# Kernel optimization log

Hardware: AMD Instinct MI355X
Metric: run time of the kernel (lower is better)

## Reference

```python
import jax, jax.numpy as jnp
import numpy as np


def _fft_feats(x):
    # x: [B, 3, H, W] float32
    B, C, H, W = x.shape
    gray = 0.299 * x[:, 0] + 0.587 * x[:, 1] + 0.114 * x[:, 2]  # [B,H,W]
    mag = jnp.abs(jnp.fft.fftshift(jnp.fft.fft2(gray), axes=(-2, -1))) + 1e-8
    mag = mag / (mag.max(axis=(-2, -1), keepdims=True) + 1e-8)
    m = mag.reshape(B, -1)
    n = m.shape[1]
    mean = m.mean(axis=1)
    std = jnp.clip(jnp.std(m, axis=1, ddof=1), 1e-8, None)  # torch unbiased std
    mx = m.max(axis=1)
    mn = m.min(axis=1)
    gt_mean = (m > mean[:, None]).astype(jnp.float32).mean(axis=1)
    # torch.median returns the lower of the two middle values for even n
    med = jnp.sort(m, axis=1)[:, (n - 1) // 2]
    q1 = mag[:, : H // 4].mean(axis=(1, 2))
    q2 = mag[:, H // 4 : H // 2].mean(axis=(1, 2))
    q3 = mag[:, H // 2 : 3 * H // 4].mean(axis=(1, 2))
    q4 = mag[:, 3 * H // 4 :].mean(axis=(1, 2))
    gt_half = (m > 0.5).astype(jnp.float32).mean(axis=1)
    gt_tenth = (m > 0.1).astype(jnp.float32).mean(axis=1)
    feats = jnp.stack([mean, std, mx, mn, gt_mean, med, q1, q2, q3, q4, gt_half, gt_tenth], axis=1)
    return jnp.clip(feats, -10.0, 10.0)  # [B,12]


def _bn(h, gamma, beta):
    # BatchNorm1d, training-mode forward (batch statistics, biased var), eps=1e-5
    mu = h.mean(axis=0)
    var = h.var(axis=0)
    return gamma * (h - mu) / jnp.sqrt(var + 1e-5) + beta


def _mlp(f, W1, b1, g1, be1, W2, b2, g2, be2, W3, b3):
    h = jax.nn.relu(_bn(f @ W1 + b1, g1, be1))  # Dropout(0.1) treated as identity (eval)
    h = jax.nn.relu(_bn(h @ W2 + b2, g2, be2))
    return h @ W3 + b3


def setup_inputs() -> dict:
    key = jax.random.key(0)
    ks = jax.random.split(key, 8)
    B, H, W = 64, 512, 512
    D = 512  # output_dim
    x = jax.random.normal(ks[0], (B, 3, H, W), dtype=jnp.float32)
    W1 = jax.random.normal(ks[1], (12, 64), dtype=jnp.float32) * 0.2
    b1 = jnp.zeros((64,), jnp.float32)
    g1 = jnp.ones((64,), jnp.float32)
    be1 = jnp.zeros((64,), jnp.float32)
    W2 = jax.random.normal(ks[2], (64, 128), dtype=jnp.float32) * 0.1
    b2 = jnp.zeros((128,), jnp.float32)
    g2 = jnp.ones((128,), jnp.float32)
    be2 = jnp.zeros((128,), jnp.float32)
    W3 = jax.random.normal(ks[3], (128, D), dtype=jnp.float32) * 0.08
    b3 = jnp.zeros((D,), jnp.float32)
    return {"x": x, "W1": W1, "b1": b1, "g1": g1, "be1": be1,
            "W2": W2, "b2": b2, "g2": g2, "be2": be2, "W3": W3, "b3": b3}


def reference(x, W1, b1, g1, be1, W2, b2, g2, be2, W3, b3):
    feats = _fft_feats(x)
    return _mlp(feats, W1, b1, g1, be1, W2, b2, g2, be2, W3, b3)
```

## Files before the change

kernel.cpp:

```cpp
#include <hip/hip_runtime.h>
#include <math.h>

#ifndef M_PI
#define M_PI 3.14159265358979323846
#endif

#define BB 64
#define HH 512
#define WW 512
#define NPIX (HH*WW)
#define MED_K 131072u
#define MAGB 131584
#define BSTRIDE 264
#define SS 520

__device__ __forceinline__ float wredf(float v){
  #pragma unroll
  for (int o = 32; o > 0; o >>= 1) v += __shfl_down(v, o, 64);
  return v;
}
__device__ __forceinline__ float wred_min(float v){
  #pragma unroll
  for (int o = 32; o > 0; o >>= 1) v = fminf(v, __shfl_down(v, o, 64));
  return v;
}
__device__ __forceinline__ float wred_max(float v){
  #pragma unroll
  for (int o = 32; o > 0; o >>= 1) v = fmaxf(v, __shfl_down(v, o, 64));
  return v;
}
__device__ __forceinline__ unsigned wred_addu(unsigned v){
  #pragma unroll
  for (int o = 32; o > 0; o >>= 1) v += __shfl_down(v, o, 64);
  return v;
}
__device__ __forceinline__ float wred_add_all(float v){
  #pragma unroll
  for (int o = 32; o > 0; o >>= 1) v += __shfl_xor(v, o, 64);
  return v;
}

__global__ void init_kernel(float2* __restrict__ twg, unsigned* __restrict__ scal){
  int t = threadIdx.x;
  double a = -2.0 * M_PI * (double)t / 512.0;
  twg[t] = make_float2((float)cos(a), (float)sin(a));
  #pragma unroll
  for (int q = 0; q < 8; ++q){
    int w = t*8 + q;
    scal[w] = (w >= 64 && w < 128) ? 0xFFFFFFFFu : 0u;
  }
}

__device__ __forceinline__ void build_twid(float2* T, const float2* __restrict__ twg,
                                           int t, int nthr){
  for (int i = t; i < 510; i += nthr){
    int v = i + 2;
    int z = 31 - __clz(v);
    T[i] = twg[(v - (1 << z)) << (8 - z)];
  }
}

__device__ __forceinline__ void wave_fft512(float (&re)[8], float (&im)[8],
                                            const float2* T, int lane){
  {
    const int d = 1;
    bool hi = (lane & d) != 0;
    #pragma unroll
    for (int r = 0; r < 8; ++r){
      float pre = __shfl_xor(re[r], d, 64);
      float pim = __shfl_xor(im[r], d, 64);
      float ur = hi ? pre : re[r], ui = hi ? pim : im[r];
      float vr = hi ? re[r] : pre, vi = hi ? im[r] : pim;
      re[r] = hi ? ur - vr : ur + vr;
      im[r] = hi ? ui - vi : ui + vi;
    }
  }
  #pragma unroll
  for (int st = 2; st <= 6; ++st){
    const int d = 1 << (st - 1);
    float2 w = T[((1 << (st - 1)) - 2) + (lane & (d - 1))];
    bool hi = (lane & d) != 0;
    #pragma unroll
    for (int r = 0; r < 8; ++r){
      float pre = __shfl_xor(re[r], d, 64);
      float pim = __shfl_xor(im[r], d, 64);
      float ur = hi ? pre : re[r], ui = hi ? pim : im[r];
      float rr = hi ? re[r] : pre, ri = hi ? im[r] : pim;
      float vr = w.x*rr - w.y*ri;
      float vi = w.x*ri + w.y*rr;
      re[r] = hi ? ur - vr : ur + vr;
      im[r] = hi ? ui - vi : ui + vi;
    }
  }
  {
    float2 w = T[62 + lane];
    #pragma unroll
    for (int r = 0; r < 8; r += 2){
      float vr = w.x*re[r+1] - w.y*im[r+1];
      float vi = w.x*im[r+1] + w.y*re[r+1];
      float ur = re[r], ui = im[r];
      re[r]   = ur + vr; im[r]   = ui + vi;
      re[r+1] = ur - vr; im[r+1] = ui - vi;
    }
  }
  {
    float2 w0 = T[126 + lane];
    float2 w1 = T[190 + lane];
    #pragma unroll
    for (int rb = 0; rb < 8; rb += 4){
      {
        float vr = w0.x*re[rb+2] - w0.y*im[rb+2];
        float vi = w0.x*im[rb+2] + w0.y*re[rb+2];
        float ur = re[rb], ui = im[rb];
        re[rb]   = ur + vr; im[rb]   = ui + vi;
        re[rb+2] = ur - vr; im[rb+2] = ui - vi;
      }
      {
        float vr = w1.x*re[rb+3] - w1.y*im[rb+3];
        float vi = w1.x*im[rb+3] + w1.y*re[rb+3];
        float ur = re[rb+1], ui = im[rb+1];
        re[rb+1] = ur + vr; im[rb+1] = ui + vi;
        re[rb+3] = ur - vr; im[rb+3] = ui - vi;
      }
    }
  }
  {
    #pragma unroll
    for (int r = 0; r < 4; ++r){
      float2 w = T[254 + 64*r + lane];
      float vr = w.x*re[r+4] - w.y*im[r+4];
      float vi = w.x*im[r+4] + w.y*re[r+4];
      float ur = re[r], ui = im[r];
      re[r]   = ur + vr; im[r]   = ui + vi;
      re[r+4] = ur - vr; im[r+4] = ui - vi;
    }
  }
}

__global__ __launch_bounds__(256) void row_fft_kernel(const float* __restrict__ x,
                                                      const float2* __restrict__ twg,
                                                      float2* __restrict__ out){
  __shared__ float2 T[510];
  int t = threadIdx.x;
  build_twid(T, twg, t, 256);
  __syncthreads();
  int lane = t & 63, wv = t >> 6;
  int pair = blockIdx.x*4 + wv;
  int b = pair >> 8, hp = pair & 255;
  int c0 = lane << 3;
  const float* p0 = x + (size_t)b*3*NPIX + (size_t)(2*hp)*WW + c0;
  const float* p1 = p0 + WW;
  float4 ra0 = *(const float4*)(p0);          float4 ra1 = *(const float4*)(p0+4);
  float4 ga0 = *(const float4*)(p0+NPIX);     float4 ga1 = *(const float4*)(p0+NPIX+4);
  float4 ba0 = *(const float4*)(p0+2*NPIX);   float4 ba1 = *(const float4*)(p0+2*NPIX+4);
  float4 rb0 = *(const float4*)(p1);          float4 rb1 = *(const float4*)(p1+4);
  float4 gb0 = *(const float4*)(p1+NPIX);     float4 gb1 = *(const float4*)(p1+NPIX+4);
  float4 bb0 = *(const float4*)(p1+2*NPIX);   float4 bb1 = *(const float4*)(p1+2*NPIX+4);
  float g0[8] = {0.299f*ra0.x + 0.587f*ga0.x + 0.114f*ba0.x,
                 0.299f*ra0.y + 0.587f*ga0.y + 0.114f*ba0.y,
                 0.299f*ra0.z + 0.587f*ga0.z + 0.114f*ba0.z,
                 0.299f*ra0.w + 0.587f*ga0.w + 0.114f*ba0.w,
                 0.299f*ra1.x + 0.587f*ga1.x + 0.114f*ba1.x,
                 0.299f*ra1.y + 0.587f*ga1.y + 0.114f*ba1.y,
                 0.299f*ra1.z + 0.587f*ga1.z + 0.114f*ba1.z,
                 0.299f*ra1.w + 0.587f*ga1.w + 0.114f*ba1.w};
  float g1[8] = {0.299f*rb0.x + 0.587f*gb0.x + 0.114f*bb0.x,
                 0.299f*rb0.y + 0.587f*gb0.y + 0.114f*bb0.y,
                 0.299f*rb0.z + 0.587f*gb0.z + 0.114f*bb0.z,
                 0.299f*rb0.w + 0.587f*gb0.w + 0.114f*bb0.w,
                 0.299f*rb1.x + 0.587f*gb1.x + 0.114f*bb1.x,
                 0.299f*rb1.y + 0.587f*gb1.y + 0.114f*bb1.y,
                 0.299f*rb1.z + 0.587f*gb1.z + 0.114f*bb1.z,
                 0.299f*rb1.w + 0.587f*gb1.w + 0.114f*bb1.w};
  int src = (int)(__brev((unsigned)lane) >> 26);
  float re[8], im[8];
  re[0] = __shfl(g0[0], src, 64); re[1] = __shfl(g0[4], src, 64);
  re[2] = __shfl(g0[2], src, 64); re[3] = __shfl(g0[6], src, 64);
  re[4] = __shfl(g0[1], src, 64); re[5] = __shfl(g0[5], src, 64);
  re[6] = __shfl(g0[3], src, 64); re[7] = __shfl(g0[7], src, 64);
  im[0] = __shfl(g1[0], src, 64); im[1] = __shfl(g1[4], src, 64);
  im[2] = __shfl(g1[2], src, 64); im[3] = __shfl(g1[6], src, 64);
  im[4] = __shfl(g1[1], src, 64); im[5] = __shfl(g1[5], src, 64);
  im[6] = __shfl(g1[3], src, 64); im[7] = __shfl(g1[7], src, 64);
  wave_fft512(re, im, T, lane);
  int row0 = (b << 9) + 2*hp;
  float2* o0 = out + (size_t)row0*BSTRIDE;
  float2* o1 = o0 + BSTRIDE;
  int srcl = (64 - lane) & 63;
  float p4r = __shfl(re[4], srcl, 64), p4i = __shfl(im[4], srcl, 64);
  float p5r = __shfl(re[5], srcl, 64), p5i = __shfl(im[5], srcl, 64);
  float p6r = __shfl(re[6], srcl, 64), p6i = __shfl(im[6], srcl, 64);
  float p7r = __shfl(re[7], srcl, 64), p7i = __shfl(im[7], srcl, 64);
  bool l0 = (lane == 0);
  {
    float zr = re[0], zi = im[0];
    float wr = l0 ? re[0] : p7r, wi = l0 ? im[0] : p7i;
    o0[lane] = make_float2(0.5f*(zr + wr), 0.5f*(zi - wi));
    o1[lane] = make_float2(0.5f*(zi + wi), 0.5f*(wr - zr));
  }
  {
    float zr = re[1], zi = im[1];
    float wr = l0 ? re[7] : p6r, wi = l0 ? im[7] : p6i;
    int k = lane + 64;
    o0[k] = make_float2(0.5f*(zr + wr), 0.5f*(zi - wi));
    o1[k] = make_float2(0.5f*(zi + wi), 0.5f*(wr - zr));
  }
  {
    float zr = re[2], zi = im[2];
    float wr = l0 ? re[6] : p5r, wi = l0 ? im[6] : p5i;
    int k = lane + 128;
    o0[k] = make_float2(0.5f*(zr + wr), 0.5f*(zi - wi));
    o1[k] = make_float2(0.5f*(zi + wi), 0.5f*(wr - zr));
  }
  {
    float zr = re[3], zi = im[3];
    float wr = l0 ? re[5] : p4r, wi = l0 ? im[5] : p4i;
    int k = lane + 192;
    o0[k] = make_float2(0.5f*(zr + wr), 0.5f*(zi - wi));
    o1[k] = make_float2(0.5f*(zi + wi), 0.5f*(wr - zr));
  }
  if (l0){
    float zr = re[4], zi = im[4];
    o0[256] = make_float2(zr, 0.f);
    o1[256] = make_float2(zi, 0.f);
  }
}

__global__ __launch_bounds__(512) void col_fft_kernel(const float2* __restrict__ in,
    const float2* __restrict__ twg,
    float* __restrict__ magc,
    unsigned* __restrict__ dmax, unsigned* __restrict__ dmin,
    double* __restrict__ sum, double* __restrict__ sumsq, double* __restrict__ qsum,
    unsigned* __restrict__ hist1)
{
  __shared__ float st_re[8*SS];
  __shared__ float st_im[8*SS];
  __shared__ float2 T[510];
  __shared__ unsigned h[8*256];
  __shared__ float buff[8][8];
  int t = threadIdx.x;
  int lane = t & 63, wv = t >> 6;
  build_twid(T, twg, t, 512);
  for (int i = t; i < 2048; i += 512) h[i] = 0u;
  int b = blockIdx.x / 33;
  int j0 = (blockIdx.x % 33) << 3;
  const float2* base = in + (size_t)b * (size_t)(512*BSTRIDE);
  #pragma unroll
  for (int it = 0; it < 8; ++it){
    int idx = t + (it << 9);
    int e = idx >> 3, jj = idx & 7;
    float2 v = base[(size_t)e*BSTRIDE + j0 + jj];
    int se = e ^ (e >> 3);
    st_re[jj*SS + se] = v.x;
    st_im[jj*SS + se] = v.y;
  }
  __syncthreads();
  int j = j0 + wv;
  if (j <= 256){
    int K = (int)(__brev((unsigned)lane) >> 26);
    const int rv3[8] = {0,4,2,6,1,5,3,7};
    float re[8], im[8];
    #pragma unroll
    for (int r = 0; r < 8; ++r){
      int e = 8*K + rv3[r];
      int se = e ^ K;
      re[r] = st_re[wv*SS + se];
      im[r] = st_im[wv*SS + se];
    }
    wave_fft512(re, im, T, lane);
    unsigned wu = (j == 0 || j == 256) ? 1u : 2u;
    float* mo = magc + (size_t)b*MAGB + (size_t)j*512;
    unsigned* hw = h + (wv << 8);
    float lsum=0.f, lsq=0.f, lq0=0.f, lq1=0.f, lq2=0.f, lq3=0.f;
    float lmn = 3.4e38f, lmx = 0.f;
    #pragma unroll
    for (int r = 0; r < 8; ++r){
      float m = sqrtf(re[r]*re[r] + im[r]*im[r]) + 1e-8f;
      int k = lane + 64*r;
      int si = (k + 256) & 511;
      mo[si] = m;
      float wm = (wu == 2u) ? m + m : m;
      lsum += wm;
      lsq = fmaf(wm, m, lsq);
      lmn = fminf(lmn, m); lmx = fmaxf(lmx, m);
      atomicAdd(&hw[__float_as_uint(m) >> 23], wu);
      int qa = si >> 7;
      lq0 += (qa==0)?m:0.f; lq1 += (qa==1)?m:0.f; lq2 += (qa==2)?m:0.f; lq3 += (qa==3)?m:0.f;
      if (wu == 2u){
        int qb = si ? 3 - ((si-1) >> 7) : 0;
        lq0 += (qb==0)?m:0.f; lq1 += (qb==1)?m:0.f; lq2 += (qb==2)?m:0.f; lq3 += (qb==3)?m:0.f;
      }
    }
    float r0 = wredf(lsum), r1 = wredf(lsq);
    float r2 = wredf(lq0), r3 = wredf(lq1), r4 = wredf(lq2), r5 = wredf(lq3);
    float fmn = wred_min(lmn), fmx = wred_max(lmx);
    if (lane == 0){
      buff[0][wv]=r0; buff[1][wv]=r1; buff[2][wv]=r2;
      buff[3][wv]=r3; buff[4][wv]=r4; buff[5][wv]=r5;
      buff[6][wv]=fmn; buff[7][wv]=fmx;
    }
  }
  __syncthreads();
  int nact = 257 - j0; if (nact > 8) nact = 8;
  if (t == 0){
    double s0=0,s1=0,s2=0,s3=0,s4=0,s5=0; float mn=3.4e38f, mx=0.f;
    for (int i = 0; i < nact; ++i){
      s0+=(double)buff[0][i]; s1+=(double)buff[1][i]; s2+=(double)buff[2][i];
      s3+=(double)buff[3][i]; s4+=(double)buff[4][i]; s5+=(double)buff[5][i];
      mn=fminf(mn,buff[6][i]); mx=fmaxf(mx,buff[7][i]);
    }
    atomicAdd(sum + b, s0);
    atomicAdd(sumsq + b, s1);
    atomicAdd(qsum + b*4 + 0, s2);
    atomicAdd(qsum + b*4 + 1, s3);
    atomicAdd(qsum + b*4 + 2, s4);
    atomicAdd(qsum + b*4 + 3, s5);
    atomicMin(dmin + b, __float_as_uint(mn));
    atomicMax(dmax + b, __float_as_uint(mx));
  }
  unsigned* hb = hist1 + (size_t)b*256;
  if (t < 256){
    unsigned c = h[t] + h[256+t] + h[512+t] + h[768+t]
               + h[1024+t] + h[1280+t] + h[1536+t] + h[1792+t];
    if (c) atomicAdd(&hb[t], c);
  }
}

__global__ __launch_bounds__(256) void pass2_kernel(const float4* __restrict__ magc4,
    const unsigned* __restrict__ hist1, const double* __restrict__ sum,
    const unsigned* __restrict__ dmax,
    unsigned* __restrict__ hist2, unsigned* __restrict__ cnt_gtm,
    unsigned* __restrict__ cnt_half, unsigned* __restrict__ cnt_tenth)
{
  __shared__ unsigned h[16384];
  __shared__ unsigned part[256];
  __shared__ unsigned rb[3][4];
  __shared__ unsigned s_sel;
  int t = threadIdx.x, b = blockIdx.x;
  for (int i = t; i < 16384; i += 256) h[i] = 0;
  const unsigned* hb1 = hist1 + (size_t)b*256;
  part[t] = hb1[t];
  __syncthreads();
  if (t == 0){
    unsigned target = MED_K, cum = 0; int bin = 0;
    for (; bin < 256; ++bin){ if (cum + part[bin] >= target) break; cum += part[bin]; }
    s_sel = (unsigned)bin;
  }
  __syncthreads();
  unsigned s1 = s_sel;
  float meanf = (float)(sum[b] / (double)NPIX);
  float d = __uint_as_float(dmax[b]) + 1e-8f;
  float th = 0.5f*d, tl = 0.1f*d;
  int c_lo = blockIdx.y * 65;
  int ncols = 257 - c_lo; if (ncols > 65) ncols = 65;
  const float4* p = magc4 + (size_t)b*(MAGB/4) + (size_t)c_lo*128;
  unsigned lgm = 0, lh = 0, lt = 0;
  int n4 = ncols * 128;
  for (int idx = t; idx < n4; idx += 256){
    float4 v = p[idx];
    int col = c_lo + (idx >> 7);
    unsigned w = (col == 0 || col == 256) ? 1u : 2u;
    float a[4] = {v.x, v.y, v.z, v.w};
    #pragma unroll
    for (int q = 0; q < 4; ++q){
      float m = a[q];
      unsigned bits = __float_as_uint(m);
      if ((bits >> 23) == s1) atomicAdd(&h[(bits >> 9) & 0x3fffu], w);
      lgm += (m > meanf) ? w : 0u;
      lh  += (m > th) ? w : 0u;
      lt  += (m > tl) ? w : 0u;
    }
  }
  int lane = t & 63, wv = t >> 6;
  unsigned g0 = wred_addu(lgm), g1 = wred_addu(lh), g2 = wred_addu(lt);
  if (lane == 0){ rb[0][wv]=g0; rb[1][wv]=g1; rb[2][wv]=g2; }
  __syncthreads();
  if (t == 0){
    unsigned a0=0,a1=0,a2=0;
    for (int i = 0; i < 4; ++i){ a0+=rb[0][i]; a1+=rb[1][i]; a2+=rb[2][i]; }
    atomicAdd(cnt_gtm + b, a0);
    atomicAdd(cnt_half + b, a1);
    atomicAdd(cnt_tenth + b, a2);
  }
  unsigned* hb = hist2 + (size_t)b*16384;
  for (int i = t; i < 16384; i += 256){
    unsigned c = h[i];
    if (c) atomicAdd(&hb[i], c);
  }
}

__global__ __launch_bounds__(256) void scan2_feats_kernel(
    const unsigned* __restrict__ hist1, const unsigned* __restrict__ hist2,
    const unsigned* __restrict__ dmax, const unsigned* __restrict__ dmin,
    const double* __restrict__ sum, const double* __restrict__ sumsq,
    const double* __restrict__ qsum,
    const unsigned* __restrict__ cnt_half, const unsigned* __restrict__ cnt_tenth,
    const unsigned* __restrict__ cnt_gtmean,
    float* __restrict__ feats)
{
  int b = blockIdx.x, t = threadIdx.x;
  __shared__ unsigned part[256];
  __shared__ unsigned s_sel, s_rem;
  const unsigned* hb1 = hist1 + (size_t)b*256;
  part[t] = hb1[t];
  __syncthreads();
  if (t == 0){
    unsigned target = MED_K, cum = 0; int bin = 0;
    for (; bin < 256; ++bin){ if (cum + part[bin] >= target) break; cum += part[bin]; }
    s_sel = (unsigned)bin; s_rem = target - cum;
  }
  __syncthreads();
  const unsigned* hb2 = hist2 + (size_t)b*16384;
  {
    unsigned sp = 0;
    for (int i = 0; i < 64; ++i) sp += hb2[t*64 + i];
    part[t] = sp;
  }
  __syncthreads();
  if (t == 0){
    unsigned target = s_rem, cum = 0; int seg = 0;
    for (; seg < 256; ++seg){ if (cum + part[seg] >= target) break; cum += part[seg]; }
    unsigned r = target - cum;
    int bin = seg*64;
    for (;; ++bin){ unsigned c = hb2[bin]; if (c >= r) break; r -= c; }
    unsigned medbits = (s_sel << 23) | ((unsigned)bin << 9) | 256u;
    float maxv = __uint_as_float(dmax[b]);
    float dd_f = maxv + 1e-8f;
    double dd = (double)dd_f;
    double n = (double)NPIX;
    double sm = sum[b] / dd;
    double sq = sumsq[b] / (dd*dd);
    double mean = sm / n;
    double var = (sq - sm*sm/n) / (n - 1.0);
    if (var < 0.0) var = 0.0;
    float stdv = (float)sqrt(var);
    if (stdv < 1e-8f) stdv = 1e-8f;
    float f[12];
    f[0] = (float)mean;
    f[1] = stdv;
    f[2] = maxv / dd_f;
    f[3] = __uint_as_float(dmin[b]) / dd_f;
    f[4] = (float)((double)cnt_gtmean[b] / n);
    f[5] = __uint_as_float(medbits) / dd_f;
    f[6] = (float)(qsum[b*4+0] / dd * (1.0/65536.0));
    f[7] = (float)(qsum[b*4+1] / dd * (1.0/65536.0));
    f[8] = (float)(qsum[b*4+2] / dd * (1.0/65536.0));
    f[9] = (float)(qsum[b*4+3] / dd * (1.0/65536.0));
    f[10] = (float)((double)cnt_half[b] / n);
    f[11] = (float)((double)cnt_tenth[b] / n);
    #pragma unroll
    for (int i = 0; i < 12; ++i)
      feats[b*12 + i] = fminf(fmaxf(f[i], -10.f), 10.f);
  }
}

__global__ __launch_bounds__(64) void mlp1_kernel(const float* __restrict__ feats,
    const float* __restrict__ W1, const float* __restrict__ b1,
    const float* __restrict__ g1, const float* __restrict__ be1,
    float* __restrict__ h1t)
{
  int c = blockIdx.x, r = threadIdx.x;
  float acc = b1[c];
  #pragma unroll
  for (int k = 0; k < 12; ++k) acc += feats[r*12 + k] * W1[k*64 + c];
  float mu = wred_add_all(acc) * (1.f/BB);
  float dv = acc - mu;
  float var = wred_add_all(dv*dv) * (1.f/BB);
  float scv = g1[c] / sqrtf(var + 1e-5f);
  float v = dv*scv + be1[c];
  h1t[c*BB + r] = v > 0.f ? v : 0.f;
}

__global__ __launch_bounds__(64) void mlp2_kernel(const float* __restrict__ h1t,
    const float* __restrict__ W2, const float* __restrict__ b2,
    const float* __restrict__ g2, const float* __restrict__ be2,
    float* __restrict__ h2t)
{
  int c = blockIdx.x, r = threadIdx.x;
  float acc = b2[c];
  #pragma unroll 4
  for (int k = 0; k < 64; ++k) acc += h1t[k*BB + r] * W2[k*128 + c];
  float mu = wred_add_all(acc) * (1.f/BB);
  float dv = acc - mu;
  float var = wred_add_all(dv*dv) * (1.f/BB);
  float scv = g2[c] / sqrtf(var + 1e-5f);
  float v = dv*scv + be2[c];
  h2t[c*BB + r] = v > 0.f ? v : 0.f;
}

__global__ __launch_bounds__(256) void mlp3_kernel(const float* __restrict__ h2t,
    const float* __restrict__ W3, const float* __restrict__ b3,
    float* __restrict__ out)
{
  int r = threadIdx.x & 63;
  int w = threadIdx.x >> 6;
  int c = blockIdx.x*4 + w;
  float acc = b3[c];
  #pragma unroll 4
  for (int k = 0; k < 128; ++k) acc += h2t[k*BB + r] * W3[k*512 + c];
  out[r*512 + c] = acc;
}

extern "C" void kernel_launch(void* const* d_in, const int* in_sizes, int n_in,
                              void* d_out, int out_size, void* d_ws, size_t ws_size,
                              hipStream_t stream) {
  (void)in_sizes; (void)n_in; (void)out_size; (void)ws_size;
  const float* x   = (const float*)d_in[0];
  const float* W1  = (const float*)d_in[1];
  const float* b1  = (const float*)d_in[2];
  const float* g1  = (const float*)d_in[3];
  const float* be1 = (const float*)d_in[4];
  const float* W2  = (const float*)d_in[5];
  const float* b2  = (const float*)d_in[6];
  const float* g2  = (const float*)d_in[7];
  const float* be2 = (const float*)d_in[8];
  const float* W3  = (const float*)d_in[9];
  const float* b3  = (const float*)d_in[10];
  float* out = (float*)d_out;

  char* ws = (char*)d_ws;
  float2* bufc = (float2*)ws;
  float*  magc = (float*)(ws + 134217728);
  unsigned* hist1 = (unsigned*)(ws + 134217728 + 34078720);
  unsigned* hist2 = (unsigned*)(ws + 168296448 + 65536);
  char* sc = ws + 168361984 + 4194304;
  unsigned* dmax      = (unsigned*)(sc + 0);
  unsigned* dmin      = (unsigned*)(sc + 256);
  double*   sum       = (double*)(sc + 512);
  double*   sumsq     = (double*)(sc + 1024);
  double*   qsum      = (double*)(sc + 1536);
  unsigned* cnt_half  = (unsigned*)(sc + 3584);
  unsigned* cnt_tenth = (unsigned*)(sc + 3840);
  unsigned* cnt_gtm   = (unsigned*)(sc + 4096);
  float*    feats     = (float*)(sc + 5120);
  float*    h1t       = (float*)(sc + 8192);
  float*    h2t       = (float*)(sc + 8192 + 16384);
  float2*   twg       = (float2*)(sc + 8192 + 16384 + 32768);

  hipMemsetAsync(hist1, 0, 65536 + 4194304, stream);

  init_kernel<<<1, 256, 0, stream>>>(twg, (unsigned*)sc);
  row_fft_kernel<<<BB*64, 256, 0, stream>>>(x, twg, bufc);
  col_fft_kernel<<<BB*33, 512, 0, stream>>>(bufc, twg, magc, dmax, dmin, sum, sumsq, qsum, hist1);
  pass2_kernel<<<dim3(BB, 4), 256, 0, stream>>>((const float4*)magc, hist1, sum, dmax,
      hist2, cnt_gtm, cnt_half, cnt_tenth);
  scan2_feats_kernel<<<BB, 256, 0, stream>>>(hist1, hist2, dmax, dmin, sum, sumsq, qsum,
      cnt_half, cnt_tenth, cnt_gtm, feats);
  mlp1_kernel<<<64, 64, 0, stream>>>(feats, W1, b1, g1, be1, h1t);
  mlp2_kernel<<<128, 64, 0, stream>>>(h1t, W2, b2, g2, be2, h2t);
  mlp3_kernel<<<128, 256, 0, stream>>>(h2t, W3, b3, out);
}
```

Measured before the change: 441.7 us.

## Write per-slice median histograms directly and reduce them in scan, simplify FFT butterflies

pass2 now writes each block's 16K-bin shared histogram straight to its own global slice with vector stores, replacing sparse global atomics. scan2 sums the four slices into shared memory before searching. This shrinks the workspace memset to cover only hist1. The FFT butterfly stages become select-free coefficient arithmetic, and the column-kernel quadrant accumulation uses compile-time indices in place of per-element compares. The trade-off is a larger workspace and extra global reads in scan2 in exchange for removing atomics and most of the memset.

Measured after the change: 441.3 us. No clear change (-0.1%).

```diff
diff --git a/kernel.cpp b/kernel.cpp
--- a/kernel.cpp
+++ b/kernel.cpp
@@ -60,19 +60,28 @@
   }
 }
 
+__device__ __forceinline__ void bfly_stage(float (&re)[8], float (&im)[8],
+                                           int d, float A, float B, float C, float D){
+  #pragma unroll
+  for (int r = 0; r < 8; ++r){
+    float ore = __shfl_xor(re[r], d, 64);
+    float oim = __shfl_xor(im[r], d, 64);
+    float sre = re[r], sim = im[r];
+    re[r] = A*sre + B*ore + C*sim + D*oim;
+    im[r] = A*sim + B*oim - C*sre - D*ore;
+  }
+}
+
 __device__ __forceinline__ void wave_fft512(float (&re)[8], float (&im)[8],
                                             const float2* T, int lane){
   {
-    const int d = 1;
-    bool hi = (lane & d) != 0;
+    float A = (lane & 1) ? -1.f : 1.f;
     #pragma unroll
     for (int r = 0; r < 8; ++r){
-      float pre = __shfl_xor(re[r], d, 64);
-      float pim = __shfl_xor(im[r], d, 64);
-      float ur = hi ? pre : re[r], ui = hi ? pim : im[r];
-      float vr = hi ? re[r] : pre, vi = hi ? im[r] : pim;
-      re[r] = hi ? ur - vr : ur + vr;
-      im[r] = hi ? ui - vi : ui + vi;
+      float ore = __shfl_xor(re[r], 1, 64);
+      float oim = __shfl_xor(im[r], 1, 64);
+      re[r] = A*re[r] + ore;
+      im[r] = A*im[r] + oim;
     }
   }
   #pragma unroll
@@ -80,17 +89,11 @@
     const int d = 1 << (st - 1);
     float2 w = T[((1 << (st - 1)) - 2) + (lane & (d - 1))];
     bool hi = (lane & d) != 0;
-    #pragma unroll
-    for (int r = 0; r < 8; ++r){
-      float pre = __shfl_xor(re[r], d, 64);
-      float pim = __shfl_xor(im[r], d, 64);
-      float ur = hi ? pre : re[r], ui = hi ? pim : im[r];
-      float rr = hi ? re[r] : pre, ri = hi ? im[r] : pim;
-      float vr = w.x*rr - w.y*ri;
-      float vi = w.x*ri + w.y*rr;
-      re[r] = hi ? ur - vr : ur + vr;
-      im[r] = hi ? ui - vi : ui + vi;
-    }
+    float A = hi ? -w.x : 1.f;
+    float B = hi ? 1.f : w.x;
+    float C = hi ? w.y : 0.f;
+    float D = hi ? 0.f : -w.y;
+    bfly_stage(re, im, d, A, B, C, D);
   }
   {
     float2 w = T[62 + lane];
@@ -271,28 +274,34 @@
     unsigned wu = (j == 0 || j == 256) ? 1u : 2u;
     float* mo = magc + (size_t)b*MAGB + (size_t)j*512;
     unsigned* hw = h + (wv << 8);
-    float lsum=0.f, lsq=0.f, lq0=0.f, lq1=0.f, lq2=0.f, lq3=0.f;
+    float lsum=0.f, lsq=0.f;
+    float lq[4] = {0.f, 0.f, 0.f, 0.f};
     float lmn = 3.4e38f, lmx = 0.f;
+    const int QA[8]  = {2,2,3,3,0,0,1,1};
+    const int QBM[8] = {1,1,0,0,3,3,2,2};
     #pragma unroll
     for (int r = 0; r < 8; ++r){
       float m = sqrtf(re[r]*re[r] + im[r]*im[r]) + 1e-8f;
-      int k = lane + 64*r;
-      int si = (k + 256) & 511;
-      mo[si] = m;
+      const int basei = 64*((r+4)&7);
+      mo[basei + lane] = m;
       float wm = (wu == 2u) ? m + m : m;
       lsum += wm;
       lsq = fmaf(wm, m, lsq);
       lmn = fminf(lmn, m); lmx = fmaxf(lmx, m);
       atomicAdd(&hw[__float_as_uint(m) >> 23], wu);
-      int qa = si >> 7;
-      lq0 += (qa==0)?m:0.f; lq1 += (qa==1)?m:0.f; lq2 += (qa==2)?m:0.f; lq3 += (qa==3)?m:0.f;
+      lq[QA[r]] += m;
       if (wu == 2u){
-        int qb = si ? 3 - ((si-1) >> 7) : 0;
-        lq0 += (qb==0)?m:0.f; lq1 += (qb==1)?m:0.f; lq2 += (qb==2)?m:0.f; lq3 += (qb==3)?m:0.f;
+        if ((r & 1) == 0){
+          float m0 = (lane == 0) ? m : 0.f;
+          lq[QBM[r]] += m - m0;
+          lq[(QBM[r]+1)&3] += m0;
+        } else {
+          lq[QBM[r]] += m;
+        }
       }
     }
     float r0 = wredf(lsum), r1 = wredf(lsq);
-    float r2 = wredf(lq0), r3 = wredf(lq1), r4 = wredf(lq2), r5 = wredf(lq3);
+    float r2 = wredf(lq[0]), r3 = wredf(lq[1]), r4 = wredf(lq[2]), r5 = wredf(lq[3]);
     float fmn = wred_min(lmn), fmx = wred_max(lmx);
     if (lane == 0){
       buff[0][wv]=r0; buff[1][wv]=r1; buff[2][wv]=r2;
@@ -332,12 +341,15 @@
     unsigned* __restrict__ hist2, unsigned* __restrict__ cnt_gtm,
     unsigned* __restrict__ cnt_half, unsigned* __restrict__ cnt_tenth)
 {
-  __shared__ unsigned h[16384];
+  __shared__ __align__(16) unsigned h[16384];
   __shared__ unsigned part[256];
   __shared__ unsigned rb[3][4];
   __shared__ unsigned s_sel;
   int t = threadIdx.x, b = blockIdx.x;
-  for (int i = t; i < 16384; i += 256) h[i] = 0;
+  {
+    uint4 z = make_uint4(0u,0u,0u,0u);
+    for (int i = t; i < 4096; i += 256) ((uint4*)h)[i] = z;
+  }
   const unsigned* hb1 = hist1 + (size_t)b*256;
   part[t] = hb1[t];
   __syncthreads();
@@ -382,11 +394,9 @@
     atomicAdd(cnt_half + b, a1);
     atomicAdd(cnt_tenth + b, a2);
   }
-  unsigned* hb = hist2 + (size_t)b*16384;
-  for (int i = t; i < 16384; i += 256){
-    unsigned c = h[i];
-    if (c) atomicAdd(&hb[i], c);
-  }
+  unsigned* hb = hist2 + (((size_t)b*4) + blockIdx.y)*16384;
+  for (int i = t; i < 4096; i += 256)
+    ((uint4*)hb)[i] = ((const uint4*)h)[i];
 }
 
 __global__ __launch_bounds__(256) void scan2_feats_kernel(
@@ -399,8 +409,19 @@
     float* __restrict__ feats)
 {
   int b = blockIdx.x, t = threadIdx.x;
+  __shared__ __align__(16) unsigned hsum[16384];
   __shared__ unsigned part[256];
   __shared__ unsigned s_sel, s_rem;
+  const uint4* h0 = (const uint4*)(hist2 + (size_t)b*4*16384);
+  for (int i = t; i < 4096; i += 256){
+    uint4 a = h0[i], c = h0[4096 + i], d2 = h0[8192 + i], e = h0[12288 + i];
+    uint4 s;
+    s.x = a.x + c.x + d2.x + e.x;
+    s.y = a.y + c.y + d2.y + e.y;
+    s.z = a.z + c.z + d2.z + e.z;
+    s.w = a.w + c.w + d2.w + e.w;
+    ((uint4*)hsum)[i] = s;
+  }
   const unsigned* hb1 = hist1 + (size_t)b*256;
   part[t] = hb1[t];
   __syncthreads();
@@ -410,10 +431,10 @@
     s_sel = (unsigned)bin; s_rem = target - cum;
   }
   __syncthreads();
-  const unsigned* hb2 = hist2 + (size_t)b*16384;
   {
     unsigned sp = 0;
-    for (int i = 0; i < 64; ++i) sp += hb2[t*64 + i];
+    int basei = t*64;
+    for (int i = 0; i < 64; ++i) sp += hsum[basei + ((i + t) & 63)];
     part[t] = sp;
   }
   __syncthreads();
@@ -422,7 +443,7 @@
     for (; seg < 256; ++seg){ if (cum + part[seg] >= target) break; cum += part[seg]; }
     unsigned r = target - cum;
     int bin = seg*64;
-    for (;; ++bin){ unsigned c = hb2[bin]; if (c >= r) break; r -= c; }
+    for (;; ++bin){ unsigned c = hsum[bin]; if (c >= r) break; r -= c; }
     unsigned medbits = (s_sel << 23) | ((unsigned)bin << 9) | 256u;
     float maxv = __uint_as_float(dmax[b]);
     float dd_f = maxv + 1e-8f;
@@ -523,7 +544,7 @@
   float*  magc = (float*)(ws + 134217728);
   unsigned* hist1 = (unsigned*)(ws + 134217728 + 34078720);
   unsigned* hist2 = (unsigned*)(ws + 168296448 + 65536);
-  char* sc = ws + 168361984 + 4194304;
+  char* sc = ws + 168361984 + 16777216;
   unsigned* dmax      = (unsigned*)(sc + 0);
   unsigned* dmin      = (unsigned*)(sc + 256);
   double*   sum       = (double*)(sc + 512);
@@ -537,7 +558,7 @@
   float*    h2t       = (float*)(sc + 8192 + 16384);
   float2*   twg       = (float2*)(sc + 8192 + 16384 + 32768);
 
-  hipMemsetAsync(hist1, 0, 65536 + 4194304, stream);
+  hipMemsetAsync(hist1, 0, 65536, stream);
 
   init_kernel<<<1, 256, 0, stream>>>(twg, (unsigned*)sc);
   row_fft_kernel<<<BB*64, 256, 0, stream>>>(x, twg, bufc);
```
